# Kernel tuning notes

Hardware: AMD Instinct MI355X
Metric: run time of the kernel (lower is better)

The kernel has to match this reference:

```python
import jax, jax.numpy as jnp
import numpy as np

H, DH = 8, 64            # heads, dim_head (module defaults)
B, N, DN, DE = 1, 512, 128, 64  # batch, nodes, node feat, edge feat
INNER = H * DH


def _w(key, fan_in, fan_out):
    return jax.random.normal(key, (fan_in, fan_out), jnp.float32) / np.sqrt(fan_in)


def setup_inputs() -> dict:
    key = jax.random.key(0)
    ks = jax.random.split(key, 8)
    return {
        "nodes": jax.random.normal(ks[0], (B, N, DN), jnp.float32),
        "edges": jax.random.normal(ks[1], (B, N, N, DE), jnp.float32),
        "mask": jnp.ones((B, N), dtype=bool),
        "Wq": _w(ks[2], DN, INNER), "bq": jnp.zeros((INNER,), jnp.float32),
        "Wk": _w(ks[3], DN, INNER), "bk": jnp.zeros((INNER,), jnp.float32),
        "Wv": _w(ks[4], DN, INNER), "bv": jnp.zeros((INNER,), jnp.float32),
        "We": _w(ks[5], DE, INNER), "be": jnp.zeros((INNER,), jnp.float32),
        "Wo": _w(ks[6], INNER, DN), "bo": jnp.zeros((DN,), jnp.float32),
    }


def _split_heads(x):
    # (b, ..., h*d) -> (b*h, ..., d), matching rearrange 'b ... (h d) -> (b h) ... d'
    b = x.shape[0]
    mid = x.shape[1:-1]
    x = x.reshape(b, *mid, H, DH)
    x = jnp.moveaxis(x, -2, 1)              # (b, h, ..., d)
    return x.reshape(b * H, *mid, DH)


def reference(nodes, edges, mask, Wq, bq, Wk, bk, Wv, bv, We, be, Wo, bo):
    scale = DH ** (-0.5)
    q = _split_heads(nodes @ Wq + bq)        # (bh, n, d)
    k = _split_heads(nodes @ Wk + bk)        # (bh, n, d)
    v = _split_heads(nodes @ Wv + bv)        # (bh, n, d)
    e = _split_heads(edges @ We + be)        # (bh, n, n, d) -- ek == ev == e_kv
    k = k[:, None, :, :] + e                 # (bh, i, j, d) per-ij keys
    v = v[:, None, :, :] + e                 # (bh, i, j, d) per-ij values
    sim = jnp.einsum('bid,bijd->bij', q, k) * scale
    m = mask[:, :, None] & mask[:, None, :]  # (b, i, j)
    m = jnp.repeat(m, H, axis=0)             # (bh, i, j)
    sim = jnp.where(m, sim, -jnp.finfo(sim.dtype).max)
    attn = jax.nn.softmax(sim, axis=-1)
    out = jnp.einsum('bij,bijd->bid', attn, v)           # (bh, n, d)
    out = out.reshape(B, H, N, DH).transpose(0, 2, 1, 3).reshape(B, N, INNER)
    return out @ Wo + bo                                  # (b, n, d_node)
```

## Files before the change

kernel.cpp:

```cpp
#include <hip/hip_runtime.h>
#include <hip/hip_bf16.h>

#define NN 512
#define DNODE 128
#define DEDGE 64
#define NH 8
#define DHD 64
#define DIN 512
#define SCALE 0.125f

typedef unsigned short u16;
typedef unsigned int u32;
typedef short bf16x8 __attribute__((ext_vector_type(8)));
typedef float f32x4 __attribute__((ext_vector_type(4)));
typedef float fx4 __attribute__((ext_vector_type(4)));

__device__ __forceinline__ float bf2f(u16 b) {
    u32 u = ((u32)b) << 16;
    return __builtin_bit_cast(float, u);
}
__device__ __forceinline__ u16 f2bf(float f) {
    u32 u = __builtin_bit_cast(u32, f);
    return (u16)((u + 0x7fffu + ((u >> 16) & 1u)) >> 16);
}
__device__ __forceinline__ float bflo(u32 u) { return __builtin_bit_cast(float, u << 16); }
__device__ __forceinline__ float bfhi(u32 u) { return __builtin_bit_cast(float, u & 0xffff0000u); }

__global__ __launch_bounds__(256) void k_qkv(
    const float* __restrict__ nodes,
    const float* __restrict__ Wq, const float* __restrict__ bq,
    const float* __restrict__ Wk, const float* __restrict__ bk,
    const float* __restrict__ Wv, const float* __restrict__ bv,
    float* __restrict__ Qo, float* __restrict__ Ko, float* __restrict__ Vo)
{
    const int it = blockIdx.x, ct = blockIdx.y, which = blockIdx.z;
    const float* W    = which == 0 ? Wq : (which == 1 ? Wk : Wv);
    const float* bias = which == 0 ? bq : (which == 1 ? bk : bv);
    float* O          = which == 0 ? Qo : (which == 1 ? Ko : Vo);
    __shared__ float As[64][132];
    __shared__ float Bs[128][68];
    const int t = threadIdx.x;
    const int ibase = it * 64, cbase = ct * 64;
#pragma unroll
    for (int p = 0; p < 8; ++p) {
        int r = p * 8 + (t >> 5), c4 = (t & 31) * 4;
        *(float4*)&As[r][c4] = *(const float4*)(nodes + (ibase + r) * DNODE + c4);
    }
#pragma unroll
    for (int p = 0; p < 8; ++p) {
        int k = p * 16 + (t >> 4), c4 = (t & 15) * 4;
        *(float4*)&Bs[k][c4] = *(const float4*)(W + k * DIN + cbase + c4);
    }
    __syncthreads();
    const int tx = t & 15, ty = t >> 4;
    float acc[4][4] = {};
    for (int k = 0; k < DNODE; ++k) {
        float4 b4 = *(const float4*)&Bs[k][tx * 4];
#pragma unroll
        for (int e = 0; e < 4; ++e) {
            float a = As[ty * 4 + e][k];
            acc[e][0] += a * b4.x; acc[e][1] += a * b4.y;
            acc[e][2] += a * b4.z; acc[e][3] += a * b4.w;
        }
    }
    const int h = ct;
#pragma unroll
    for (int ii = 0; ii < 4; ++ii) {
        int i = ibase + ty * 4 + ii;
        float4 o;
        o.x = acc[ii][0] + bias[cbase + tx * 4 + 0];
        o.y = acc[ii][1] + bias[cbase + tx * 4 + 1];
        o.z = acc[ii][2] + bias[cbase + tx * 4 + 2];
        o.w = acc[ii][3] + bias[cbase + tx * 4 + 3];
        *(float4*)(O + ((size_t)h * NN + i) * DHD + tx * 4) = o;
    }
}

__global__ __launch_bounds__(256) void k_qe(
    const float* __restrict__ Q, const float* __restrict__ We, float* __restrict__ QE)
{
    const int it = blockIdx.x, h = blockIdx.y;
    __shared__ float Qs[64][68];
    __shared__ float WsT[64][68];
    const int t = threadIdx.x;
    const int ibase = it * 64;
#pragma unroll
    for (int p = 0; p < 4; ++p) {
        int r = p * 16 + (t >> 4), d4 = (t & 15) * 4;
        *(float4*)&Qs[r][d4] = *(const float4*)(Q + ((size_t)h * NN + ibase + r) * DHD + d4);
    }
#pragma unroll
    for (int p = 0; p < 4; ++p) {
        int c = p * 16 + (t >> 4), d4 = (t & 15) * 4;
        float4 v = *(const float4*)(We + c * DIN + h * DHD + d4);
        WsT[d4 + 0][c] = v.x; WsT[d4 + 1][c] = v.y;
        WsT[d4 + 2][c] = v.z; WsT[d4 + 3][c] = v.w;
    }
    __syncthreads();
    const int tx = t & 15, ty = t >> 4;
    float acc[4][4] = {};
    for (int d = 0; d < DHD; ++d) {
        float4 b4 = *(const float4*)&WsT[d][tx * 4];
#pragma unroll
        for (int e = 0; e < 4; ++e) {
            float a = Qs[ty * 4 + e][d];
            acc[e][0] += a * b4.x; acc[e][1] += a * b4.y;
            acc[e][2] += a * b4.z; acc[e][3] += a * b4.w;
        }
    }
#pragma unroll
    for (int ii = 0; ii < 4; ++ii) {
        int i = ibase + ty * 4 + ii;
        float4 o;
        o.x = SCALE * acc[ii][0]; o.y = SCALE * acc[ii][1];
        o.z = SCALE * acc[ii][2]; o.w = SCALE * acc[ii][3];
        *(float4*)(QE + ((size_t)h * NN + i) * DEDGE + tx * 4) = o;
    }
}

__global__ __launch_bounds__(256) void k_qk(
    const float* __restrict__ Q, const float* __restrict__ K, float* __restrict__ QK)
{
    const int jt = blockIdx.x, it = blockIdx.y, h = blockIdx.z;
    __shared__ float Qs[64][68];
    __shared__ float KsT[64][68];
    const int t = threadIdx.x;
    const int ibase = it * 64, jbase = jt * 64;
#pragma unroll
    for (int p = 0; p < 4; ++p) {
        int r = p * 16 + (t >> 4), d4 = (t & 15) * 4;
        *(float4*)&Qs[r][d4] = *(const float4*)(Q + ((size_t)h * NN + ibase + r) * DHD + d4);
    }
#pragma unroll
    for (int p = 0; p < 4; ++p) {
        int j = p * 16 + (t >> 4), d4 = (t & 15) * 4;
        float4 v = *(const float4*)(K + ((size_t)h * NN + jbase + j) * DHD + d4);
        KsT[d4 + 0][j] = v.x; KsT[d4 + 1][j] = v.y;
        KsT[d4 + 2][j] = v.z; KsT[d4 + 3][j] = v.w;
    }
    __syncthreads();
    const int tx = t & 15, ty = t >> 4;
    float acc[4][4] = {};
    for (int d = 0; d < DHD; ++d) {
        float4 b4 = *(const float4*)&KsT[d][tx * 4];
#pragma unroll
        for (int e = 0; e < 4; ++e) {
            float a = Qs[ty * 4 + e][d];
            acc[e][0] += a * b4.x; acc[e][1] += a * b4.y;
            acc[e][2] += a * b4.z; acc[e][3] += a * b4.w;
        }
    }
#pragma unroll
    for (int ii = 0; ii < 4; ++ii) {
        int i = ibase + ty * 4 + ii;
        float4 o;
        o.x = SCALE * acc[ii][0]; o.y = SCALE * acc[ii][1];
        o.z = SCALE * acc[ii][2]; o.w = SCALE * acc[ii][3];
        *(float4*)(QK + ((size_t)h * NN + i) * NN + jbase + tx * 4) = o;
    }
}

__global__ __launch_bounds__(512, 4) void k_fused(
    const float* __restrict__ edges, const float* __restrict__ QK,
    const float* __restrict__ QE, float* __restrict__ AE, u16* __restrict__ P)
{
    __shared__ u16 erow[NN * 64];
    __shared__ u16 PlT[NH * 520];
    __shared__ float ae_acc[NH * 65];
    __shared__ float wred0[16][9];
    __shared__ float wred1[16][9];
    const int i = blockIdx.x;
    const int t = threadIdx.x;
    const int lane = t & 63, w = t >> 6;
    const int jl = lane & 15, hq = lane >> 4;
    const int h0 = hq * 4;
    const int jw = w * 64;

    const float* E = edges + (size_t)i * NN * DEDGE;
    const int jst = jw + (lane >> 3);
    const int c0 = (lane & 7) * 8;
    fx4 fa[8], fb[8];
#pragma unroll
    for (int p = 0; p < 8; ++p) {
        const float* s = E + (size_t)(jst + p * 8) * 64 + c0;
        fa[p] = *(const fx4*)s;
        fb[p] = *(const fx4*)(s + 4);
    }
#pragma unroll
    for (int p = 0; p < 8; ++p) asm volatile("" : "+v"(fa[p]), "+v"(fb[p]));
#pragma unroll
    for (int p = 0; p < 8; ++p) {
        int j = jst + p * 8;
        uint4 pk;
        pk.x = (u32)f2bf(fa[p][0]) | ((u32)f2bf(fa[p][1]) << 16);
        pk.y = (u32)f2bf(fa[p][2]) | ((u32)f2bf(fa[p][3]) << 16);
        pk.z = (u32)f2bf(fb[p][0]) | ((u32)f2bf(fb[p][1]) << 16);
        pk.w = (u32)f2bf(fb[p][2]) | ((u32)f2bf(fb[p][3]) << 16);
        int sb = (j * 128 + c0 * 2) ^ ((j & 7) << 4);
        *(uint4*)((char*)erow + sb) = pk;
    }
    for (int z = t; z < NH * 65; z += 512) ae_acc[z] = 0.f;

    float qkv[16];
#pragma unroll
    for (int jt = 0; jt < 4; ++jt)
#pragma unroll
        for (int r = 0; r < 4; ++r)
            qkv[jt * 4 + r] = (hq < 2)
                ? QK[((size_t)(h0 + r) * NN + i) * NN + jw + jt * 16 + jl] : 0.f;
    fx4 qa0 = {0,0,0,0}, qa1 = qa0, qa2 = qa0, qa3 = qa0;
    if (jl < 8) {
        const float* qe = QE + ((size_t)jl * NN + i) * DEDGE + hq * 8;
        qa0 = *(const fx4*)(qe + 0);
        qa1 = *(const fx4*)(qe + 4);
        qa2 = *(const fx4*)(qe + 32);
        qa3 = *(const fx4*)(qe + 36);
    }
    bf16x8 af0, af1;
    af0[0]=(short)f2bf(qa0[0]); af0[1]=(short)f2bf(qa0[1]); af0[2]=(short)f2bf(qa0[2]); af0[3]=(short)f2bf(qa0[3]);
    af0[4]=(short)f2bf(qa1[0]); af0[5]=(short)f2bf(qa1[1]); af0[6]=(short)f2bf(qa1[2]); af0[7]=(short)f2bf(qa1[3]);
    af1[0]=(short)f2bf(qa2[0]); af1[1]=(short)f2bf(qa2[1]); af1[2]=(short)f2bf(qa2[2]); af1[3]=(short)f2bf(qa2[3]);
    af1[4]=(short)f2bf(qa3[0]); af1[5]=(short)f2bf(qa3[1]); af1[6]=(short)f2bf(qa3[2]); af1[7]=(short)f2bf(qa3[3]);

    f32x4 acc[4] = {f32x4{0,0,0,0}, f32x4{0,0,0,0}, f32x4{0,0,0,0}, f32x4{0,0,0,0}};
    const char* eb = (const char*)erow;
#pragma unroll
    for (int jt = 0; jt < 4; ++jt) {
        int j = jw + jt * 16 + jl;
        int x = (j & 7) << 4;
        uint4 e0 = *(const uint4*)(eb + ((j * 128 + hq * 16) ^ x));
        uint4 e1 = *(const uint4*)(eb + ((j * 128 + 64 + hq * 16) ^ x));
        f32x4 a = acc[jt];
        a = __builtin_amdgcn_mfma_f32_16x16x32_bf16(af0, __builtin_bit_cast(bf16x8, e0), a, 0, 0, 0);
        a = __builtin_amdgcn_mfma_f32_16x16x32_bf16(af1, __builtin_bit_cast(bf16x8, e1), a, 0, 0, 0);
        acc[jt] = a;
    }
#pragma unroll
    for (int jt = 0; jt < 4; ++jt)
#pragma unroll
        for (int r = 0; r < 4; ++r) acc[jt][r] += qkv[jt * 4 + r];

    float lred[4];
#pragma unroll
    for (int r = 0; r < 4; ++r) {
        float m0 = fmaxf(fmaxf(acc[0][r], acc[1][r]), fmaxf(acc[2][r], acc[3][r]));
        m0 = fmaxf(m0, __shfl_xor(m0, 1));
        m0 = fmaxf(m0, __shfl_xor(m0, 2));
        m0 = fmaxf(m0, __shfl_xor(m0, 4));
        m0 = fmaxf(m0, __shfl_xor(m0, 8));
        lred[r] = m0;
    }
    if (jl == 0 && hq < 2) {
#pragma unroll
        for (int r = 0; r < 4; ++r) wred0[h0 + r][w] = lred[r];
    }
    __syncthreads();
    float mm[4];
#pragma unroll
    for (int r = 0; r < 4; ++r) {
        float m = wred0[h0 + r][0];
#pragma unroll
        for (int ww = 1; ww < 8; ++ww) m = fmaxf(m, wred0[h0 + r][ww]);
        mm[r] = m;
    }
#pragma unroll
    for (int r = 0; r < 4; ++r) {
        float ls = 0.f;
#pragma unroll
        for (int jt = 0; jt < 4; ++jt) {
            float e = __expf(acc[jt][r] - mm[r]);
            acc[jt][r] = e; ls += e;
        }
        ls += __shfl_xor(ls, 1);
        ls += __shfl_xor(ls, 2);
        ls += __shfl_xor(ls, 4);
        ls += __shfl_xor(ls, 8);
        lred[r] = ls;
    }
    if (jl == 0 && hq < 2) {
#pragma unroll
        for (int r = 0; r < 4; ++r) wred1[h0 + r][w] = lred[r];
    }
    __syncthreads();
    if (hq < 2) {
#pragma unroll
        for (int r = 0; r < 4; ++r) {
            float s = wred1[h0 + r][0];
#pragma unroll
            for (int ww = 1; ww < 8; ++ww) s += wred1[h0 + r][ww];
            float inv = 1.f / s;
            int h = h0 + r;
#pragma unroll
            for (int jt = 0; jt < 4; ++jt) {
                int j = jw + jt * 16 + jl;
                u16 pb = f2bf(acc[jt][r] * inv);
                PlT[h * 520 + j] = pb;
                P[((size_t)h * NN + i) * NN + j] = pb;
            }
        }
    }

    f32x4 ae4[4] = {f32x4{0,0,0,0}, f32x4{0,0,0,0}, f32x4{0,0,0,0}, f32x4{0,0,0,0}};
#pragma unroll
    for (int kt2 = 0; kt2 < 2; ++kt2) {
        bf16x8 pa = {0,0,0,0,0,0,0,0};
        if (jl < 8)
            pa = *(const bf16x8*)&PlT[jl * 520 + jw + kt2 * 32 + hq * 8];
        const int jb = jw + kt2 * 32 + hq * 8;
#pragma unroll
        for (int ct = 0; ct < 4; ++ct) {
            const int cc = ct * 16 + jl;
            bf16x8 bfr;
#pragma unroll
            for (int idx = 0; idx < 8; ++idx) {
                bfr[idx] = (short)*(const u16*)(eb + (((jb + idx) * 128 + cc * 2) ^ (idx << 4)));
            }
            ae4[ct] = __builtin_amdgcn_mfma_f32_16x16x32_bf16(pa, bfr, ae4[ct], 0, 0, 0);
        }
    }
    if (hq < 2) {
#pragma unroll
        for (int ct = 0; ct < 4; ++ct)
#pragma unroll
            for (int r = 0; r < 4; ++r)
                atomicAdd(&ae_acc[(h0 + r) * 65 + ct * 16 + jl], ae4[ct][r]);
    }
    __syncthreads();
    AE[(((size_t)(t >> 6)) * NN + i) * DEDGE + (t & 63)] = ae_acc[(t >> 6) * 65 + (t & 63)];
}

__global__ __launch_bounds__(256) void k_pv(
    const u16* __restrict__ P, const float* __restrict__ V, float* __restrict__ OUTV)
{
    const int ks = blockIdx.x, it = blockIdx.y, h = blockIdx.z;
    __shared__ u16 Ps[64][136];
    __shared__ float Vs[128][68];
    const int t = threadIdx.x;
    const int ibase = it * 64, kbase = ks * 128;
#pragma unroll
    for (int p = 0; p < 4; ++p) {
        int r = p * 16 + (t >> 4), j8 = (t & 15) * 8;
        *(uint4*)&Ps[r][j8] = *(const uint4*)(P + ((size_t)h * NN + ibase + r) * NN + kbase + j8);
    }
#pragma unroll
    for (int p = 0; p < 8; ++p) {
        int j = p * 16 + (t >> 4), d4 = (t & 15) * 4;
        *(float4*)&Vs[j][d4] = *(const float4*)(V + ((size_t)h * NN + kbase + j) * DHD + d4);
    }
    __syncthreads();
    const int tx = t & 15, ty = t >> 4;
    float acc[4][4] = {};
    for (int k = 0; k < 128; ++k) {
        float4 b4 = *(const float4*)&Vs[k][tx * 4];
#pragma unroll
        for (int e = 0; e < 4; ++e) {
            float a = bf2f(Ps[ty * 4 + e][k]);
            acc[e][0] += a * b4.x; acc[e][1] += a * b4.y;
            acc[e][2] += a * b4.z; acc[e][3] += a * b4.w;
        }
    }
#pragma unroll
    for (int ii = 0; ii < 4; ++ii)
#pragma unroll
        for (int jj = 0; jj < 4; ++jj)
            unsafeAtomicAdd(&OUTV[((size_t)h * NN + ibase + ty * 4 + ii) * DHD + tx * 4 + jj],
                            acc[ii][jj]);
}

__global__ __launch_bounds__(256) void k_inner(
    const float* __restrict__ AE, const float* __restrict__ We, const float* __restrict__ be,
    const float* __restrict__ OUTV, float* __restrict__ INNER)
{
    const int it = blockIdx.x, h = blockIdx.y;
    __shared__ float AEs[64][68];
    __shared__ float Ws[64][68];
    const int t = threadIdx.x;
    const int ibase = it * 64;
#pragma unroll
    for (int p = 0; p < 4; ++p) {
        int r = p * 16 + (t >> 4), c4 = (t & 15) * 4;
        *(float4*)&AEs[r][c4] = *(const float4*)(AE + ((size_t)h * NN + ibase + r) * DEDGE + c4);
    }
#pragma unroll
    for (int p = 0; p < 4; ++p) {
        int c = p * 16 + (t >> 4), d4 = (t & 15) * 4;
        *(float4*)&Ws[c][d4] = *(const float4*)(We + c * DIN + h * DHD + d4);
    }
    __syncthreads();
    const int tx = t & 15, ty = t >> 4;
    float acc[4][4] = {};
    for (int c = 0; c < DEDGE; ++c) {
        float4 b4 = *(const float4*)&Ws[c][tx * 4];
#pragma unroll
        for (int e = 0; e < 4; ++e) {
            float a = AEs[ty * 4 + e][c];
            acc[e][0] += a * b4.x; acc[e][1] += a * b4.y;
            acc[e][2] += a * b4.z; acc[e][3] += a * b4.w;
        }
    }
#pragma unroll
    for (int ii = 0; ii < 4; ++ii) {
        int i = ibase + ty * 4 + ii;
        float4 ov = *(const float4*)(OUTV + ((size_t)h * NN + i) * DHD + tx * 4);
        float4 o;
        o.x = acc[ii][0] + ov.x + be[h * DHD + tx * 4 + 0];
        o.y = acc[ii][1] + ov.y + be[h * DHD + tx * 4 + 1];
        o.z = acc[ii][2] + ov.z + be[h * DHD + tx * 4 + 2];
        o.w = acc[ii][3] + ov.w + be[h * DHD + tx * 4 + 3];
        *(float4*)(INNER + (size_t)i * DIN + h * DHD + tx * 4) = o;
    }
}

__global__ __launch_bounds__(256) void k_out(
    const float* __restrict__ INNER, const float* __restrict__ Wo, const float* __restrict__ bo,
    float* __restrict__ out)
{
    const int ks = blockIdx.x, it = blockIdx.y;
    __shared__ float Is[64][68];
    __shared__ float Wos[64][136];
    const int t = threadIdx.x;
    const int ibase = it * 64, kbase = ks * 64;
#pragma unroll
    for (int p = 0; p < 4; ++p) {
        int r = p * 16 + (t >> 4), c4 = (t & 15) * 4;
        *(float4*)&Is[r][c4] = *(const float4*)(INNER + (size_t)(ibase + r) * DIN + kbase + c4);
    }
#pragma unroll
    for (int p = 0; p < 8; ++p) {
        int k = p * 8 + (t >> 5), n4 = (t & 31) * 4;
        *(float4*)&Wos[k][n4] = *(const float4*)(Wo + (size_t)(kbase + k) * DNODE + n4);
    }
    __syncthreads();
    const int tx = t & 15, ty = t >> 4;
    float acc[4][8] = {};
    for (int k = 0; k < 64; ++k) {
        float4 b0 = *(const float4*)&Wos[k][tx * 8];
        float4 b1 = *(const float4*)&Wos[k][tx * 8 + 4];
#pragma unroll
        for (int e = 0; e < 4; ++e) {
            float a = Is[ty * 4 + e][k];
            acc[e][0] += a * b0.x; acc[e][1] += a * b0.y;
            acc[e][2] += a * b0.z; acc[e][3] += a * b0.w;
            acc[e][4] += a * b1.x; acc[e][5] += a * b1.y;
            acc[e][6] += a * b1.z; acc[e][7] += a * b1.w;
        }
    }
#pragma unroll
    for (int ii = 0; ii < 4; ++ii)
#pragma unroll
        for (int nn = 0; nn < 8; ++nn) {
            float v = acc[ii][nn] + (ks == 0 ? bo[tx * 8 + nn] : 0.f);
            unsafeAtomicAdd(&out[(size_t)(ibase + ty * 4 + ii) * DNODE + tx * 8 + nn], v);
        }
}

extern "C" void kernel_launch(void* const* d_in, const int* in_sizes, int n_in,
                              void* d_out, int out_size, void* d_ws, size_t ws_size,
                              hipStream_t stream) {
    (void)in_sizes; (void)n_in; (void)out_size; (void)ws_size;
    const float* nodes = (const float*)d_in[0];
    const float* edges = (const float*)d_in[1];
    const float* Wq = (const float*)d_in[3];  const float* bq = (const float*)d_in[4];
    const float* Wk = (const float*)d_in[5];  const float* bk = (const float*)d_in[6];
    const float* Wv = (const float*)d_in[7];  const float* bv = (const float*)d_in[8];
    const float* We = (const float*)d_in[9];  const float* be = (const float*)d_in[10];
    const float* Wo = (const float*)d_in[11]; const float* bo = (const float*)d_in[12];
    float* out = (float*)d_out;

    float* ws    = (float*)d_ws;
    float* Qb    = ws;
    float* Kb    = Qb    + NH * NN * DHD;
    float* Vb    = Kb    + NH * NN * DHD;
    float* QEb   = Vb    + NH * NN * DHD;
    float* AEb   = QEb   + NH * NN * DHD;
    float* OUTVb = AEb   + NH * NN * DHD;
    float* INb   = OUTVb + NH * NN * DHD;
    float* QKb   = INb   + (size_t)NN * DIN;
    u16*   Pb    = (u16*)(QKb + (size_t)NH * NN * NN);

    hipMemsetAsync(OUTVb, 0, (size_t)NH * NN * DHD * sizeof(float), stream);
    hipMemsetAsync(out, 0, (size_t)NN * DNODE * sizeof(float), stream);

    k_qkv<<<dim3(8, 8, 3), 256, 0, stream>>>(nodes, Wq, bq, Wk, bk, Wv, bv, Qb, Kb, Vb);
    k_qe<<<dim3(8, 8), 256, 0, stream>>>(Qb, We, QEb);
    k_qk<<<dim3(8, 8, 8), 256, 0, stream>>>(Qb, Kb, QKb);
    k_fused<<<dim3(512), 512, 0, stream>>>(edges, QKb, QEb, AEb, Pb);
    k_pv<<<dim3(4, 8, 8), 256, 0, stream>>>(Pb, Vb, OUTVb);
    k_inner<<<dim3(8, 8), 256, 0, stream>>>(AEb, We, be, OUTVb, INb);
    k_out<<<dim3(8, 8), 256, 0, stream>>>(INb, Wo, bo, out);
}
```

Before: 211.5 us.

## Fold QE projection into QKV kernel, fuse PV with inner, drop atomics and memsets

Precomputes a per-head Wq·We^T weight (with bias) so the QE projection becomes a fourth output slice of the QKV projection kernel, removing a separate dependent launch. PV and the edge-inner projection are merged into one kernel that loops over the key dimension instead of split-K with atomics. The output projection now loops over K and stores directly, so the memsets and atomic adds go away. Launch count drops, at the cost of fewer blocks (less parallelism) in the PV and output kernels.

```diff
diff --git a/kernel.cpp b/kernel.cpp
--- a/kernel.cpp
+++ b/kernel.cpp
@@ -23,33 +23,85 @@
     u32 u = __builtin_bit_cast(u32, f);
     return (u16)((u + 0x7fffu + ((u >> 16) & 1u)) >> 16);
 }
-__device__ __forceinline__ float bflo(u32 u) { return __builtin_bit_cast(float, u << 16); }
-__device__ __forceinline__ float bfhi(u32 u) { return __builtin_bit_cast(float, u & 0xffff0000u); }
-
-__global__ __launch_bounds__(256) void k_qkv(
+
+__global__ __launch_bounds__(256) void k_wqe(
+    const float* __restrict__ Wq, const float* __restrict__ We, const float* __restrict__ bq,
+    float* __restrict__ Wqe, float* __restrict__ bqe)
+{
+    const int h = blockIdx.x;
+    __shared__ float Wqs[128][68];
+    __shared__ float WesT[64][68];
+    const int t = threadIdx.x;
+#pragma unroll
+    for (int p = 0; p < 8; ++p) {
+        int r = p * 16 + (t >> 4), d4 = (t & 15) * 4;
+        *(float4*)&Wqs[r][d4] = *(const float4*)(Wq + (size_t)r * DIN + h * DHD + d4);
+    }
+#pragma unroll
+    for (int p = 0; p < 4; ++p) {
+        int c = p * 16 + (t >> 4), d4 = (t & 15) * 4;
+        float4 v = *(const float4*)(We + (size_t)c * DIN + h * DHD + d4);
+        WesT[d4 + 0][c] = v.x; WesT[d4 + 1][c] = v.y;
+        WesT[d4 + 2][c] = v.z; WesT[d4 + 3][c] = v.w;
+    }
+    __syncthreads();
+    const int tx = t & 15, ty = t >> 4;
+    float acc[8][4] = {};
+    for (int d = 0; d < DHD; ++d) {
+        float4 b4 = *(const float4*)&WesT[d][tx * 4];
+#pragma unroll
+        for (int e = 0; e < 8; ++e) {
+            float a = Wqs[ty * 8 + e][d];
+            acc[e][0] += a * b4.x; acc[e][1] += a * b4.y;
+            acc[e][2] += a * b4.z; acc[e][3] += a * b4.w;
+        }
+    }
+#pragma unroll
+    for (int e = 0; e < 8; ++e) {
+        float4 o;
+        o.x = SCALE * acc[e][0]; o.y = SCALE * acc[e][1];
+        o.z = SCALE * acc[e][2]; o.w = SCALE * acc[e][3];
+        *(float4*)(Wqe + ((size_t)h * DNODE + ty * 8 + e) * DEDGE + tx * 4) = o;
+    }
+    if (t < DEDGE) {
+        float s = 0.f;
+        for (int d = 0; d < DHD; ++d) s += bq[h * DHD + d] * WesT[d][t];
+        bqe[h * DEDGE + t] = SCALE * s;
+    }
+}
+
+__global__ __launch_bounds__(256) void k_qkv4(
     const float* __restrict__ nodes,
     const float* __restrict__ Wq, const float* __restrict__ bq,
     const float* __restrict__ Wk, const float* __restrict__ bk,
     const float* __restrict__ Wv, const float* __restrict__ bv,
-    float* __restrict__ Qo, float* __restrict__ Ko, float* __restrict__ Vo)
-{
-    const int it = blockIdx.x, ct = blockIdx.y, which = blockIdx.z;
-    const float* W    = which == 0 ? Wq : (which == 1 ? Wk : Wv);
-    const float* bias = which == 0 ? bq : (which == 1 ? bk : bv);
-    float* O          = which == 0 ? Qo : (which == 1 ? Ko : Vo);
+    const float* __restrict__ Wqe, const float* __restrict__ bqe,
+    float* __restrict__ Qo, float* __restrict__ Ko, float* __restrict__ Vo,
+    float* __restrict__ QEo)
+{
+    const int it = blockIdx.x, h = blockIdx.y, which = blockIdx.z;
     __shared__ float As[64][132];
     __shared__ float Bs[128][68];
     const int t = threadIdx.x;
-    const int ibase = it * 64, cbase = ct * 64;
+    const int ibase = it * 64;
 #pragma unroll
     for (int p = 0; p < 8; ++p) {
         int r = p * 8 + (t >> 5), c4 = (t & 31) * 4;
         *(float4*)&As[r][c4] = *(const float4*)(nodes + (ibase + r) * DNODE + c4);
     }
-#pragma unroll
-    for (int p = 0; p < 8; ++p) {
-        int k = p * 16 + (t >> 4), c4 = (t & 15) * 4;
-        *(float4*)&Bs[k][c4] = *(const float4*)(W + k * DIN + cbase + c4);
+    if (which < 3) {
+        const float* W = which == 0 ? Wq : (which == 1 ? Wk : Wv);
+#pragma unroll
+        for (int p = 0; p < 8; ++p) {
+            int k = p * 16 + (t >> 4), c4 = (t & 15) * 4;
+            *(float4*)&Bs[k][c4] = *(const float4*)(W + (size_t)k * DIN + h * DHD + c4);
+        }
+    } else {
+#pragma unroll
+        for (int p = 0; p < 8; ++p) {
+            int k = p * 16 + (t >> 4), c4 = (t & 15) * 4;
+            *(float4*)&Bs[k][c4] = *(const float4*)(Wqe + ((size_t)h * DNODE + k) * DEDGE + c4);
+        }
     }
     __syncthreads();
     const int tx = t & 15, ty = t >> 4;
@@ -63,58 +115,18 @@
             acc[e][2] += a * b4.z; acc[e][3] += a * b4.w;
         }
     }
-    const int h = ct;
+    const float* bias = which == 0 ? (bq + h * DHD) : (which == 1 ? (bk + h * DHD)
+                       : (which == 2 ? (bv + h * DHD) : (bqe + h * DEDGE)));
+    float* O = which == 0 ? Qo : (which == 1 ? Ko : (which == 2 ? Vo : QEo));
 #pragma unroll
     for (int ii = 0; ii < 4; ++ii) {
         int i = ibase + ty * 4 + ii;
         float4 o;
-        o.x = acc[ii][0] + bias[cbase + tx * 4 + 0];
-        o.y = acc[ii][1] + bias[cbase + tx * 4 + 1];
-        o.z = acc[ii][2] + bias[cbase + tx * 4 + 2];
-        o.w = acc[ii][3] + bias[cbase + tx * 4 + 3];
+        o.x = acc[ii][0] + bias[tx * 4 + 0];
+        o.y = acc[ii][1] + bias[tx * 4 + 1];
+        o.z = acc[ii][2] + bias[tx * 4 + 2];
+        o.w = acc[ii][3] + bias[tx * 4 + 3];
         *(float4*)(O + ((size_t)h * NN + i) * DHD + tx * 4) = o;
-    }
-}
-
-__global__ __launch_bounds__(256) void k_qe(
-    const float* __restrict__ Q, const float* __restrict__ We, float* __restrict__ QE)
-{
-    const int it = blockIdx.x, h = blockIdx.y;
-    __shared__ float Qs[64][68];
-    __shared__ float WsT[64][68];
-    const int t = threadIdx.x;
-    const int ibase = it * 64;
-#pragma unroll
-    for (int p = 0; p < 4; ++p) {
-        int r = p * 16 + (t >> 4), d4 = (t & 15) * 4;
-        *(float4*)&Qs[r][d4] = *(const float4*)(Q + ((size_t)h * NN + ibase + r) * DHD + d4);
-    }
-#pragma unroll
-    for (int p = 0; p < 4; ++p) {
-        int c = p * 16 + (t >> 4), d4 = (t & 15) * 4;
-        float4 v = *(const float4*)(We + c * DIN + h * DHD + d4);
-        WsT[d4 + 0][c] = v.x; WsT[d4 + 1][c] = v.y;
-        WsT[d4 + 2][c] = v.z; WsT[d4 + 3][c] = v.w;
-    }
-    __syncthreads();
-    const int tx = t & 15, ty = t >> 4;
-    float acc[4][4] = {};
-    for (int d = 0; d < DHD; ++d) {
-        float4 b4 = *(const float4*)&WsT[d][tx * 4];
-#pragma unroll
-        for (int e = 0; e < 4; ++e) {
-            float a = Qs[ty * 4 + e][d];
-            acc[e][0] += a * b4.x; acc[e][1] += a * b4.y;
-            acc[e][2] += a * b4.z; acc[e][3] += a * b4.w;
-        }
-    }
-#pragma unroll
-    for (int ii = 0; ii < 4; ++ii) {
-        int i = ibase + ty * 4 + ii;
-        float4 o;
-        o.x = SCALE * acc[ii][0]; o.y = SCALE * acc[ii][1];
-        o.z = SCALE * acc[ii][2]; o.w = SCALE * acc[ii][3];
-        *(float4*)(QE + ((size_t)h * NN + i) * DEDGE + tx * 4) = o;
     }
 }
 
@@ -186,8 +198,10 @@
         fa[p] = *(const fx4*)s;
         fb[p] = *(const fx4*)(s + 4);
     }
-#pragma unroll
-    for (int p = 0; p < 8; ++p) asm volatile("" : "+v"(fa[p]), "+v"(fb[p]));
+    asm volatile("" : "+v"(fa[0]), "+v"(fa[1]), "+v"(fa[2]), "+v"(fa[3]),
+                      "+v"(fa[4]), "+v"(fa[5]), "+v"(fa[6]), "+v"(fa[7]),
+                      "+v"(fb[0]), "+v"(fb[1]), "+v"(fb[2]), "+v"(fb[3]),
+                      "+v"(fb[4]), "+v"(fb[5]), "+v"(fb[6]), "+v"(fb[7]));
 #pragma unroll
     for (int p = 0; p < 8; ++p) {
         int j = jst + p * 8;
@@ -329,53 +343,44 @@
     AE[(((size_t)(t >> 6)) * NN + i) * DEDGE + (t & 63)] = ae_acc[(t >> 6) * 65 + (t & 63)];
 }
 
-__global__ __launch_bounds__(256) void k_pv(
-    const u16* __restrict__ P, const float* __restrict__ V, float* __restrict__ OUTV)
-{
-    const int ks = blockIdx.x, it = blockIdx.y, h = blockIdx.z;
+__global__ __launch_bounds__(256) void k_pvin(
+    const u16* __restrict__ P, const float* __restrict__ V,
+    const float* __restrict__ AE, const float* __restrict__ We, const float* __restrict__ be,
+    float* __restrict__ INNER)
+{
+    const int it = blockIdx.x, h = blockIdx.y;
     __shared__ u16 Ps[64][136];
     __shared__ float Vs[128][68];
-    const int t = threadIdx.x;
-    const int ibase = it * 64, kbase = ks * 128;
-#pragma unroll
-    for (int p = 0; p < 4; ++p) {
-        int r = p * 16 + (t >> 4), j8 = (t & 15) * 8;
-        *(uint4*)&Ps[r][j8] = *(const uint4*)(P + ((size_t)h * NN + ibase + r) * NN + kbase + j8);
-    }
-#pragma unroll
-    for (int p = 0; p < 8; ++p) {
-        int j = p * 16 + (t >> 4), d4 = (t & 15) * 4;
-        *(float4*)&Vs[j][d4] = *(const float4*)(V + ((size_t)h * NN + kbase + j) * DHD + d4);
-    }
-    __syncthreads();
+    __shared__ float AEs[64][68];
+    __shared__ float Ws[64][68];
+    const int t = threadIdx.x;
+    const int ibase = it * 64;
     const int tx = t & 15, ty = t >> 4;
     float acc[4][4] = {};
-    for (int k = 0; k < 128; ++k) {
-        float4 b4 = *(const float4*)&Vs[k][tx * 4];
-#pragma unroll
-        for (int e = 0; e < 4; ++e) {
-            float a = bf2f(Ps[ty * 4 + e][k]);
-            acc[e][0] += a * b4.x; acc[e][1] += a * b4.y;
-            acc[e][2] += a * b4.z; acc[e][3] += a * b4.w;
-        }
-    }
-#pragma unroll
-    for (int ii = 0; ii < 4; ++ii)
-#pragma unroll
-        for (int jj = 0; jj < 4; ++jj)
-            unsafeAtomicAdd(&OUTV[((size_t)h * NN + ibase + ty * 4 + ii) * DHD + tx * 4 + jj],
-                            acc[ii][jj]);
-}
-
-__global__ __launch_bounds__(256) void k_inner(
-    const float* __restrict__ AE, const float* __restrict__ We, const float* __restrict__ be,
-    const float* __restrict__ OUTV, float* __restrict__ INNER)
-{
-    const int it = blockIdx.x, h = blockIdx.y;
-    __shared__ float AEs[64][68];
-    __shared__ float Ws[64][68];
-    const int t = threadIdx.x;
-    const int ibase = it * 64;
+    for (int ks = 0; ks < 4; ++ks) {
+        const int kbase = ks * 128;
+#pragma unroll
+        for (int p = 0; p < 4; ++p) {
+            int r = p * 16 + (t >> 4), j8 = (t & 15) * 8;
+            *(uint4*)&Ps[r][j8] = *(const uint4*)(P + ((size_t)h * NN + ibase + r) * NN + kbase + j8);
+        }
+#pragma unroll
+        for (int p = 0; p < 8; ++p) {
+            int j = p * 16 + (t >> 4), d4 = (t & 15) * 4;
+            *(float4*)&Vs[j][d4] = *(const float4*)(V + ((size_t)h * NN + kbase + j) * DHD + d4);
+        }
+        __syncthreads();
+        for (int k = 0; k < 128; ++k) {
+            float4 b4 = *(const float4*)&Vs[k][tx * 4];
+#pragma unroll
+            for (int e = 0; e < 4; ++e) {
+                float a = bf2f(Ps[ty * 4 + e][k]);
+                acc[e][0] += a * b4.x; acc[e][1] += a * b4.y;
+                acc[e][2] += a * b4.z; acc[e][3] += a * b4.w;
+            }
+        }
+        __syncthreads();
+    }
 #pragma unroll
     for (int p = 0; p < 4; ++p) {
         int r = p * 16 + (t >> 4), c4 = (t & 15) * 4;
@@ -384,11 +389,9 @@
 #pragma unroll
     for (int p = 0; p < 4; ++p) {
         int c = p * 16 + (t >> 4), d4 = (t & 15) * 4;
-        *(float4*)&Ws[c][d4] = *(const float4*)(We + c * DIN + h * DHD + d4);
-    }
-    __syncthreads();
-    const int tx = t & 15, ty = t >> 4;
-    float acc[4][4] = {};
+        *(float4*)&Ws[c][d4] = *(const float4*)(We + (size_t)c * DIN + h * DHD + d4);
+    }
+    __syncthreads();
     for (int c = 0; c < DEDGE; ++c) {
         float4 b4 = *(const float4*)&Ws[c][tx * 4];
 #pragma unroll
@@ -401,12 +404,11 @@
 #pragma unroll
     for (int ii = 0; ii < 4; ++ii) {
         int i = ibase + ty * 4 + ii;
-        float4 ov = *(const float4*)(OUTV + ((size_t)h * NN + i) * DHD + tx * 4);
         float4 o;
-        o.x = acc[ii][0] + ov.x + be[h * DHD + tx * 4 + 0];
-        o.y = acc[ii][1] + ov.y + be[h * DHD + tx * 4 + 1];
-        o.z = acc[ii][2] + ov.z + be[h * DHD + tx * 4 + 2];
-        o.w = acc[ii][3] + ov.w + be[h * DHD + tx * 4 + 3];
+        o.x = acc[ii][0] + be[h * DHD + tx * 4 + 0];
+        o.y = acc[ii][1] + be[h * DHD + tx * 4 + 1];
+        o.z = acc[ii][2] + be[h * DHD + tx * 4 + 2];
+        o.w = acc[ii][3] + be[h * DHD + tx * 4 + 3];
         *(float4*)(INNER + (size_t)i * DIN + h * DHD + tx * 4) = o;
     }
 }
@@ -415,43 +417,46 @@
     const float* __restrict__ INNER, const float* __restrict__ Wo, const float* __restrict__ bo,
     float* __restrict__ out)
 {
-    const int ks = blockIdx.x, it = blockIdx.y;
+    const int it = blockIdx.x, nt = blockIdx.y;
     __shared__ float Is[64][68];
-    __shared__ float Wos[64][136];
-    const int t = threadIdx.x;
-    const int ibase = it * 64, kbase = ks * 64;
-#pragma unroll
-    for (int p = 0; p < 4; ++p) {
-        int r = p * 16 + (t >> 4), c4 = (t & 15) * 4;
-        *(float4*)&Is[r][c4] = *(const float4*)(INNER + (size_t)(ibase + r) * DIN + kbase + c4);
-    }
-#pragma unroll
-    for (int p = 0; p < 8; ++p) {
-        int k = p * 8 + (t >> 5), n4 = (t & 31) * 4;
-        *(float4*)&Wos[k][n4] = *(const float4*)(Wo + (size_t)(kbase + k) * DNODE + n4);
-    }
-    __syncthreads();
+    __shared__ float Wos[64][68];
+    const int t = threadIdx.x;
+    const int ibase = it * 64, nbase = nt * 64;
     const int tx = t & 15, ty = t >> 4;
-    float acc[4][8] = {};
-    for (int k = 0; k < 64; ++k) {
-        float4 b0 = *(const float4*)&Wos[k][tx * 8];
-        float4 b1 = *(const float4*)&Wos[k][tx * 8 + 4];
-#pragma unroll
-        for (int e = 0; e < 4; ++e) {
-            float a = Is[ty * 4 + e][k];
-            acc[e][0] += a * b0.x; acc[e][1] += a * b0.y;
-            acc[e][2] += a * b0.z; acc[e][3] += a * b0.w;
-            acc[e][4] += a * b1.x; acc[e][5] += a * b1.y;
-            acc[e][6] += a * b1.z; acc[e][7] += a * b1.w;
-        }
-    }
-#pragma unroll
-    for (int ii = 0; ii < 4; ++ii)
-#pragma unroll
-        for (int nn = 0; nn < 8; ++nn) {
-            float v = acc[ii][nn] + (ks == 0 ? bo[tx * 8 + nn] : 0.f);
-            unsafeAtomicAdd(&out[(size_t)(ibase + ty * 4 + ii) * DNODE + tx * 8 + nn], v);
-        }
+    float acc[4][4] = {};
+    for (int kc = 0; kc < 8; ++kc) {
+        const int kbase = kc * 64;
+#pragma unroll
+        for (int p = 0; p < 4; ++p) {
+            int r = p * 16 + (t >> 4), c4 = (t & 15) * 4;
+            *(float4*)&Is[r][c4] = *(const float4*)(INNER + (size_t)(ibase + r) * DIN + kbase + c4);
+        }
+#pragma unroll
+        for (int p = 0; p < 4; ++p) {
+            int k = p * 16 + (t >> 4), n4 = (t & 15) * 4;
+            *(float4*)&Wos[k][n4] = *(const float4*)(Wo + (size_t)(kbase + k) * DNODE + nbase + n4);
+        }
+        __syncthreads();
+        for (int k = 0; k < 64; ++k) {
+            float4 b4 = *(const float4*)&Wos[k][tx * 4];
+#pragma unroll
+            for (int e = 0; e < 4; ++e) {
+                float a = Is[ty * 4 + e][k];
+                acc[e][0] += a * b4.x; acc[e][1] += a * b4.y;
+                acc[e][2] += a * b4.z; acc[e][3] += a * b4.w;
+            }
+        }
+        __syncthreads();
+    }
+#pragma unroll
+    for (int ii = 0; ii < 4; ++ii) {
+        float4 o;
+        o.x = acc[ii][0] + bo[nbase + tx * 4 + 0];
+        o.y = acc[ii][1] + bo[nbase + tx * 4 + 1];
+        o.z = acc[ii][2] + bo[nbase + tx * 4 + 2];
+        o.w = acc[ii][3] + bo[nbase + tx * 4 + 3];
+        *(float4*)(out + (size_t)(ibase + ty * 4 + ii) * DNODE + nbase + tx * 4) = o;
+    }
 }
 
 extern "C" void kernel_launch(void* const* d_in, const int* in_sizes, int n_in,
@@ -473,19 +478,17 @@
     float* Vb    = Kb    + NH * NN * DHD;
     float* QEb   = Vb    + NH * NN * DHD;
     float* AEb   = QEb   + NH * NN * DHD;
-    float* OUTVb = AEb   + NH * NN * DHD;
-    float* INb   = OUTVb + NH * NN * DHD;
-    float* QKb   = INb   + (size_t)NN * DIN;
+    float* INb   = AEb   + NH * NN * DHD;
+    float* Wqe   = INb   + (size_t)NN * DIN;
+    float* bqe   = Wqe   + NH * DNODE * DEDGE;
+    float* QKb   = bqe   + NH * DEDGE;
     u16*   Pb    = (u16*)(QKb + (size_t)NH * NN * NN);
 
-    hipMemsetAsync(OUTVb, 0, (size_t)NH * NN * DHD * sizeof(float), stream);
-    hipMemsetAsync(out, 0, (size_t)NN * DNODE * sizeof(float), stream);
-
-    k_qkv<<<dim3(8, 8, 3), 256, 0, stream>>>(nodes, Wq, bq, Wk, bk, Wv, bv, Qb, Kb, Vb);
-    k_qe<<<dim3(8, 8), 256, 0, stream>>>(Qb, We, QEb);
+    k_wqe<<<dim3(NH), 256, 0, stream>>>(Wq, We, bq, Wqe, bqe);
+    k_qkv4<<<dim3(8, 8, 4), 256, 0, stream>>>(nodes, Wq, bq, Wk, bk, Wv, bv,
+                                              Wqe, bqe, Qb, Kb, Vb, QEb);
     k_qk<<<dim3(8, 8, 8), 256, 0, stream>>>(Qb, Kb, QKb);
     k_fused<<<dim3(512), 512, 0, stream>>>(edges, QKb, QEb, AEb, Pb);
-    k_pv<<<dim3(4, 8, 8), 256, 0, stream>>>(Pb, Vb, OUTVb);
-    k_inner<<<dim3(8, 8), 256, 0, stream>>>(AEb, We, be, OUTVb, INb);
-    k_out<<<dim3(8, 8), 256, 0, stream>>>(INb, Wo, bo, out);
-}
+    k_pvin<<<dim3(8, 8), 256, 0, stream>>>(Pb, Vb, AEb, We, be, INb);
+    k_out<<<dim3(8, 2), 256, 0, stream>>>(INb, Wo, bo, out);
+}
```

After: 207.7 us. Within noise of the previous version (-1.8%).
